# Kernel optimization log

Hardware: AMD Instinct MI355X
Metric: run time of the kernel (lower is better)

Reference implementation:

```python
import jax, jax.numpy as jnp
import numpy as np

DEFAULT_SCORE = -10000.0


def select_with_default(nidx, score_vec, default):
    # nidx: [V, K] int, score_vec: [V] float -> [V, K] float
    gathered = score_vec[jnp.maximum(nidx, 0)]
    return jnp.where(nidx < 0, jnp.asarray(default, gathered.dtype), gathered)


def setup_inputs() -> dict:
    key = jax.random.key(0)
    k1, k2, k3 = jax.random.split(key, 3)
    V, K = 1000000, 64
    dist = jax.random.uniform(k1, (V, K), dtype=jnp.float32)
    # column 0 is the self index by convention; remaining are neighbour indices
    nbrs = jax.random.randint(k2, (V, K - 1), 0, V, dtype=jnp.int32)
    nidx = jnp.concatenate([jnp.arange(V, dtype=jnp.int32)[:, None], nbrs], axis=1)
    score = jax.random.uniform(k3, (V, 1), dtype=jnp.float32)
    return {"dist": dist, "nidx": nidx, "score": score}


def reference(dist, nidx, score):
    # neighscores: [V, K]; default -10000 for missing (-1) neighbours
    neighscores = select_with_default(nidx, score[:, 0], DEFAULT_SCORE)
    # max over real neighbours (exclude self column 0), keepdims -> [V, 1]
    diff = score - jnp.max(neighscores[:, 1:], axis=1, keepdims=True)
    # keep self index, drop all neighbours (-1) where a higher-score neighbour exists
    noneigh = jnp.concatenate(
        [nidx[:, 0:1], jnp.full_like(nidx[:, 1:], -1)], axis=-1
    )
    cond = diff < 0  # [V, 1], broadcasts over K
    dist_out = jnp.where(cond, jnp.zeros((), dist.dtype), dist)
    nidx_out = jnp.where(cond, noneigh, nidx)
    return dist_out, nidx_out
```

## Files before the change

kernel.cpp:

```cpp
#include <hip/hip_runtime.h>

#define DEFAULT_SCORE -10000.0f


typedef int   iv4 __attribute__((ext_vector_type(4)));
typedef float fv4 __attribute__((ext_vector_type(4)));

constexpr int WAVE_ROWS = 16;

__global__ __launch_bounds__(256) void dgb_kernel(
    const float* __restrict__ dist,
    const int*   __restrict__ nidx,
    const float* __restrict__ score,
    float*       __restrict__ dist_out,
    float*       __restrict__ nidx_out,
    int V) {
  const int lane = threadIdx.x & 63;
  const int wave = blockIdx.x * (blockDim.x >> 6) + (threadIdx.x >> 6);
  const int k    = lane & 3;
  const int row  = wave * WAVE_ROWS + (lane >> 2);
  const bool valid = row < V;
  const size_t rowbase = (size_t)row * 64;
  const int grp = lane & 60;

  iv4 idx1 = (iv4)(-1);
  float self = 0.0f;
  if (valid) {
    idx1 = __builtin_nontemporal_load(
        reinterpret_cast<const iv4*>(nidx + rowbase) + k);
    self = score[row];
  }
  float g0 = (idx1.x >= 0) ? score[idx1.x] : DEFAULT_SCORE;
  float g1 = (idx1.y >= 0) ? score[idx1.y] : DEFAULT_SCORE;
  float g2 = (idx1.z >= 0) ? score[idx1.z] : DEFAULT_SCORE;
  float g3 = (idx1.w >= 0) ? score[idx1.w] : DEFAULT_SCORE;
  if (k == 0) g0 = DEFAULT_SCORE;
  const bool p1 = fmaxf(fmaxf(g0, g1), fmaxf(g2, g3)) > self;
  const unsigned long long b1 = __ballot(p1);
  const bool resolved = ((b1 >> grp) & 0xFull) != 0;

  float m2 = DEFAULT_SCORE;
  if (valid && !resolved) {
#pragma unroll
    for (int j = 0; j < 3; ++j) {
      const iv4 id = __builtin_nontemporal_load(
          reinterpret_cast<const iv4*>(nidx + rowbase + 16 + j * 16) + k);
      const float h0 = (id.x >= 0) ? score[id.x] : DEFAULT_SCORE;
      const float h1 = (id.y >= 0) ? score[id.y] : DEFAULT_SCORE;
      const float h2 = (id.z >= 0) ? score[id.z] : DEFAULT_SCORE;
      const float h3 = (id.w >= 0) ? score[id.w] : DEFAULT_SCORE;
      m2 = fmaxf(m2, fmaxf(fmaxf(h0, h1), fmaxf(h2, h3)));
    }
  }
  const unsigned long long b2 = __ballot(m2 > self);
  const bool cond = resolved || (((b2 >> grp) & 0xFull) != 0);

  if (!valid) return;

#pragma unroll
  for (int j = 0; j < 4; ++j) {
    const size_t off = rowbase + (size_t)j * 16 + (size_t)k * 4;
    fv4 d4, n4;
    if (cond) {
      d4 = (fv4)(0.0f);
      const float nx = (j == 0 && k == 0) ? (float)idx1.x : -1.0f;
      n4 = (fv4){nx, -1.0f, -1.0f, -1.0f};
    } else {
      d4 = __builtin_nontemporal_load(
          reinterpret_cast<const fv4*>(dist + off));
      iv4 id;
      if (j == 0) id = idx1;
      else
        id = __builtin_nontemporal_load(
            reinterpret_cast<const iv4*>(nidx + off));
      n4 = (fv4){(float)id.x, (float)id.y, (float)id.z, (float)id.w};
    }
    __builtin_nontemporal_store(d4, reinterpret_cast<fv4*>(dist_out + off));
    __builtin_nontemporal_store(n4, reinterpret_cast<fv4*>(nidx_out + off));
  }
}

extern "C" void kernel_launch(void* const* d_in, const int* in_sizes, int n_in,
                              void* d_out, int out_size, void* d_ws, size_t ws_size,
                              hipStream_t stream) {
  const float* dist  = (const float*)d_in[0];
  const int*   nidx  = (const int*)d_in[1];
  const float* score = (const float*)d_in[2];

  const int V = in_sizes[2];

  float* dist_out = (float*)d_out;
  float* nidx_out = (float*)d_out + (size_t)V * 64;

  const int rows_per_block = (256 / 64) * WAVE_ROWS;
  const int grid = (V + rows_per_block - 1) / rows_per_block;

  dgb_kernel<<<grid, 256, 0, stream>>>(dist, nidx, score, dist_out, nidx_out, V);
}
```

Measured before the change: 927.5 us.

## Assign one row per lane with wave-level early exit over neighbour chunks

Each lane now owns a whole row and scans its neighbour indices in progressively larger chunks, skipping further chunks once every row in the wave has found a higher-scoring neighbour. The copy-out phase is then reorganised so 16 lanes cooperate on each row for coalesced stores, using a ballot mask of the per-row conditions. The aim is to cut index loads and score gathers for rows resolved early. In exchange, the index loads become strided per lane rather than coalesced, the chunks are processed serially with more dependent latency, and the wave only stops once its slowest row is resolved.

```diff
diff --git a/kernel.cpp b/kernel.cpp
--- a/kernel.cpp
+++ b/kernel.cpp
@@ -5,8 +5,6 @@
 
 typedef int   iv4 __attribute__((ext_vector_type(4)));
 typedef float fv4 __attribute__((ext_vector_type(4)));
-
-constexpr int WAVE_ROWS = 16;
 
 __global__ __launch_bounds__(256) void dgb_kernel(
     const float* __restrict__ dist,
@@ -17,66 +15,92 @@
     int V) {
   const int lane = threadIdx.x & 63;
   const int wave = blockIdx.x * (blockDim.x >> 6) + (threadIdx.x >> 6);
-  const int k    = lane & 3;
-  const int row  = wave * WAVE_ROWS + (lane >> 2);
+  const int wrow0 = wave << 6;
+
+  const int row = wrow0 + lane;
   const bool valid = row < V;
-  const size_t rowbase = (size_t)row * 64;
-  const int grp = lane & 60;
+  const size_t rb = (size_t)row << 6;
+  const iv4* rowp = reinterpret_cast<const iv4*>(nidx + rb);
 
-  iv4 idx1 = (iv4)(-1);
   float self = 0.0f;
-  if (valid) {
-    idx1 = __builtin_nontemporal_load(
-        reinterpret_cast<const iv4*>(nidx + rowbase) + k);
-    self = score[row];
+  if (valid) self = score[row];
+  bool done = !valid;
+
+  if (!done) {
+    const iv4 a = __builtin_nontemporal_load(rowp);
+    const float g1 = (a.y >= 0) ? score[a.y] : DEFAULT_SCORE;
+    const float g2 = (a.z >= 0) ? score[a.z] : DEFAULT_SCORE;
+    const float g3 = (a.w >= 0) ? score[a.w] : DEFAULT_SCORE;
+    if (fmaxf(fmaxf(g1, g2), g3) > self) done = true;
   }
-  float g0 = (idx1.x >= 0) ? score[idx1.x] : DEFAULT_SCORE;
-  float g1 = (idx1.y >= 0) ? score[idx1.y] : DEFAULT_SCORE;
-  float g2 = (idx1.z >= 0) ? score[idx1.z] : DEFAULT_SCORE;
-  float g3 = (idx1.w >= 0) ? score[idx1.w] : DEFAULT_SCORE;
-  if (k == 0) g0 = DEFAULT_SCORE;
-  const bool p1 = fmaxf(fmaxf(g0, g1), fmaxf(g2, g3)) > self;
-  const unsigned long long b1 = __ballot(p1);
-  const bool resolved = ((b1 >> grp) & 0xFull) != 0;
-
-  float m2 = DEFAULT_SCORE;
-  if (valid && !resolved) {
 #pragma unroll
-    for (int j = 0; j < 3; ++j) {
-      const iv4 id = __builtin_nontemporal_load(
-          reinterpret_cast<const iv4*>(nidx + rowbase + 16 + j * 16) + k);
-      const float h0 = (id.x >= 0) ? score[id.x] : DEFAULT_SCORE;
-      const float h1 = (id.y >= 0) ? score[id.y] : DEFAULT_SCORE;
-      const float h2 = (id.z >= 0) ? score[id.z] : DEFAULT_SCORE;
-      const float h3 = (id.w >= 0) ? score[id.w] : DEFAULT_SCORE;
-      m2 = fmaxf(m2, fmaxf(fmaxf(h0, h1), fmaxf(h2, h3)));
+  for (int c = 1; c < 4; ++c) {
+    if (__any(!done)) {
+      if (!done) {
+        const iv4 a = __builtin_nontemporal_load(rowp + c);
+        const float g0 = (a.x >= 0) ? score[a.x] : DEFAULT_SCORE;
+        const float g1 = (a.y >= 0) ? score[a.y] : DEFAULT_SCORE;
+        const float g2 = (a.z >= 0) ? score[a.z] : DEFAULT_SCORE;
+        const float g3 = (a.w >= 0) ? score[a.w] : DEFAULT_SCORE;
+        if (fmaxf(fmaxf(g0, g1), fmaxf(g2, g3)) > self) done = true;
+      }
     }
   }
-  const unsigned long long b2 = __ballot(m2 > self);
-  const bool cond = resolved || (((b2 >> grp) & 0xFull) != 0);
+#pragma unroll
+  for (int c = 1; c < 4; ++c) {
+    if (__any(!done)) {
+      if (!done) {
+        const iv4* p = rowp + 4 * c;
+        const iv4 a0 = __builtin_nontemporal_load(p);
+        const iv4 a1 = __builtin_nontemporal_load(p + 1);
+        const iv4 a2 = __builtin_nontemporal_load(p + 2);
+        const iv4 a3 = __builtin_nontemporal_load(p + 3);
+        float m = DEFAULT_SCORE;
+        m = fmaxf(m, (a0.x >= 0) ? score[a0.x] : DEFAULT_SCORE);
+        m = fmaxf(m, (a0.y >= 0) ? score[a0.y] : DEFAULT_SCORE);
+        m = fmaxf(m, (a0.z >= 0) ? score[a0.z] : DEFAULT_SCORE);
+        m = fmaxf(m, (a0.w >= 0) ? score[a0.w] : DEFAULT_SCORE);
+        m = fmaxf(m, (a1.x >= 0) ? score[a1.x] : DEFAULT_SCORE);
+        m = fmaxf(m, (a1.y >= 0) ? score[a1.y] : DEFAULT_SCORE);
+        m = fmaxf(m, (a1.z >= 0) ? score[a1.z] : DEFAULT_SCORE);
+        m = fmaxf(m, (a1.w >= 0) ? score[a1.w] : DEFAULT_SCORE);
+        m = fmaxf(m, (a2.x >= 0) ? score[a2.x] : DEFAULT_SCORE);
+        m = fmaxf(m, (a2.y >= 0) ? score[a2.y] : DEFAULT_SCORE);
+        m = fmaxf(m, (a2.z >= 0) ? score[a2.z] : DEFAULT_SCORE);
+        m = fmaxf(m, (a2.w >= 0) ? score[a2.w] : DEFAULT_SCORE);
+        m = fmaxf(m, (a3.x >= 0) ? score[a3.x] : DEFAULT_SCORE);
+        m = fmaxf(m, (a3.y >= 0) ? score[a3.y] : DEFAULT_SCORE);
+        m = fmaxf(m, (a3.z >= 0) ? score[a3.z] : DEFAULT_SCORE);
+        m = fmaxf(m, (a3.w >= 0) ? score[a3.w] : DEFAULT_SCORE);
+        if (m > self) done = true;
+      }
+    }
+  }
+  const unsigned long long cbits = __ballot(done && valid);
 
-  if (!valid) return;
+  const int sub  = lane >> 4;
+  const int col0 = (lane & 15) << 2;
+#pragma unroll 4
+  for (int s = 0; s < 16; ++s) {
+    const int r = (s << 2) + sub;
+    const int orow = wrow0 + r;
+    if (wrow0 + (s << 2) >= V) break;
+    const bool c = (cbits >> r) & 1ull;
+    const size_t off = ((size_t)orow << 6) + col0;
 
-#pragma unroll
-  for (int j = 0; j < 4; ++j) {
-    const size_t off = rowbase + (size_t)j * 16 + (size_t)k * 4;
-    fv4 d4, n4;
-    if (cond) {
-      d4 = (fv4)(0.0f);
-      const float nx = (j == 0 && k == 0) ? (float)idx1.x : -1.0f;
-      n4 = (fv4){nx, -1.0f, -1.0f, -1.0f};
-    } else {
+    fv4 d4 = (fv4)(0.0f);
+    fv4 n4 = {(col0 == 0) ? (float)orow : -1.0f, -1.0f, -1.0f, -1.0f};
+    if (orow < V && !c) {
       d4 = __builtin_nontemporal_load(
           reinterpret_cast<const fv4*>(dist + off));
-      iv4 id;
-      if (j == 0) id = idx1;
-      else
-        id = __builtin_nontemporal_load(
-            reinterpret_cast<const iv4*>(nidx + off));
+      const iv4 id = __builtin_nontemporal_load(
+          reinterpret_cast<const iv4*>(nidx + off));
       n4 = (fv4){(float)id.x, (float)id.y, (float)id.z, (float)id.w};
     }
-    __builtin_nontemporal_store(d4, reinterpret_cast<fv4*>(dist_out + off));
-    __builtin_nontemporal_store(n4, reinterpret_cast<fv4*>(nidx_out + off));
+    if (orow < V) {
+      __builtin_nontemporal_store(d4, reinterpret_cast<fv4*>(dist_out + off));
+      __builtin_nontemporal_store(n4, reinterpret_cast<fv4*>(nidx_out + off));
+    }
   }
 }
 
@@ -92,7 +116,7 @@
   float* dist_out = (float*)d_out;
   float* nidx_out = (float*)d_out + (size_t)V * 64;
 
-  const int rows_per_block = (256 / 64) * WAVE_ROWS;
+  const int rows_per_block = 4 * 64;
   const int grid = (V + rows_per_block - 1) / rows_per_block;
 
   dgb_kernel<<<grid, 256, 0, stream>>>(dist, nidx, score, dist_out, nidx_out, V);
```

Result: faster. 786.1 us (-15.2%).
